# Optimization experiments

Measured on AMD Instinct MI355X. Metric: run time of the kernel, lower is better.

## Reference

```python
import jax, jax.numpy as jnp
import numpy as np

L = 3        # num_layers
B = 8192     # batch slots
H = 1024     # hidden_dim (== decoder_in_dim)
D_IN = 1024
D_OUT = 80
N_ACT = 4096 # active rows selected by hidden_idx


def setup_inputs() -> dict:
    key = jax.random.key(0)
    ks = jax.random.split(key, 8)
    encoded = jax.random.normal(ks[0], (B, D_IN), jnp.float32)
    hidden = jax.random.normal(ks[1], (L, B, H), jnp.float32)
    hidden_idx = jnp.arange(N_ACT, dtype=jnp.int32)  # unique, in-range batch indices
    s = 0.05  # small init scale for stable gate math
    w_ih = jax.random.normal(ks[2], (L, 3 * H, D_IN), jnp.float32) * s
    w_hh = jax.random.normal(ks[3], (L, 3 * H, H), jnp.float32) * s
    b_ih = jax.random.normal(ks[4], (L, 3 * H), jnp.float32) * s
    b_hh = jax.random.normal(ks[5], (L, 3 * H), jnp.float32) * s
    w_out = jax.random.normal(ks[6], (D_OUT, H), jnp.float32) * s
    b_out = jax.random.normal(ks[7], (D_OUT,), jnp.float32) * s
    return {"encoded": encoded, "hidden": hidden, "hidden_idx": hidden_idx,
            "w_ih": w_ih, "w_hh": w_hh, "b_ih": b_ih, "b_hh": b_hh,
            "w_out": w_out, "b_out": b_out}


def reference(encoded, hidden, hidden_idx, w_ih, w_hh, b_ih, b_hh, w_out, b_out):
    # Gather active rows, run stacked GRUCells, scatter back (eval mode: dropout = identity).
    x = encoded[hidden_idx]                       # [N, D_IN]
    new_hidden = []
    for i in range(L):                            # small fixed layer loop
        h_full = hidden[i]                        # [B, H]
        h = h_full[hidden_idx]                    # [N, H]
        gi = x @ w_ih[i].T + b_ih[i]              # [N, 3H] gates from input
        gh = h @ w_hh[i].T + b_hh[i]              # [N, 3H] gates from hidden
        i_r, i_z, i_n = jnp.split(gi, 3, axis=-1)
        h_r, h_z, h_n = jnp.split(gh, 3, axis=-1)
        r = jax.nn.sigmoid(i_r + h_r)
        z = jax.nn.sigmoid(i_z + h_z)
        n = jnp.tanh(i_n + r * h_n)
        h_out = (1.0 - z) * n + z * h             # torch GRUCell update
        x = h_out
        new_hidden.append(h_full.at[hidden_idx].set(h_out))
    y = jnp.tanh(x @ w_out.T + b_out)             # linear head + tanh activation
    output = jnp.zeros((B, D_OUT), y.dtype).at[hidden_idx].set(y)
    return (output, jnp.stack(new_hidden))
```

## Files before the change

### kernel.cpp

```cpp
#include <hip/hip_runtime.h>

typedef unsigned short ushort_t;
typedef unsigned char uchar_t;
typedef unsigned int uint_t;
typedef __attribute__((ext_vector_type(8))) short bf16x8;
typedef __attribute__((ext_vector_type(4))) float f32x4;

constexpr int L_   = 3;
constexpr int B_   = 8192;
constexpr int H_   = 1024;
constexpr int DOUT_= 80;
constexpr int NACT_= 4096;
constexpr int G3_  = 3 * H_;

static __device__ __forceinline__ ushort_t f2bf(float f) {
    uint_t u = __float_as_uint(f);
    uint_t r = (u + 0x7FFFu + ((u >> 16) & 1u)) >> 16;
    return (ushort_t)r;
}

static __device__ __forceinline__ void gll16(const void* g, void* l) {
    __builtin_amdgcn_global_load_lds(
        (const __attribute__((address_space(1))) uint32_t*)g,
        (__attribute__((address_space(3))) uint32_t*)l, 16, 0, 0);
}

__global__ void prep_all(const float* __restrict__ encoded, const float* __restrict__ hidden,
                         const int* __restrict__ idx,
                         const float* __restrict__ wih, const float* __restrict__ whh,
                         const float* __restrict__ wout,
                         ushort_t* __restrict__ oih, ushort_t* __restrict__ ohh,
                         ushort_t* __restrict__ oout,
                         ushort_t* __restrict__ x0, ushort_t* __restrict__ hb,
                         uchar_t* __restrict__ mask) {
    int tid = blockIdx.x * blockDim.x + threadIdx.x;
    int nth = gridDim.x * blockDim.x;
    if (tid < NACT_) mask[idx[tid]] = 1;
    const int NW = L_ * G3_ * H_ / 4;
    for (int i = tid; i < NW; i += nth) {
        float4 a = ((const float4*)wih)[i];
        ushort4 o; o.x = f2bf(a.x); o.y = f2bf(a.y); o.z = f2bf(a.z); o.w = f2bf(a.w);
        ((ushort4*)oih)[i] = o;
        float4 b = ((const float4*)whh)[i];
        ushort4 p; p.x = f2bf(b.x); p.y = f2bf(b.y); p.z = f2bf(b.z); p.w = f2bf(b.w);
        ((ushort4*)ohh)[i] = p;
    }
    const int NO = DOUT_ * H_ / 4;
    for (int i = tid; i < NO; i += nth) {
        float4 a = ((const float4*)wout)[i];
        ushort4 o; o.x = f2bf(a.x); o.y = f2bf(a.y); o.z = f2bf(a.z); o.w = f2bf(a.w);
        ((ushort4*)oout)[i] = o;
    }
    const int C4 = H_ / 4;
    const int PER = NACT_ * C4;
    for (int i = tid; i < 4 * PER; i += nth) {
        int seg = i / PER;
        int rem = i - seg * PER;
        int r = rem / C4, c = rem % C4;
        int gr = idx[r];
        const float* src = (seg == 0) ? (encoded + (size_t)gr * H_)
                                      : (hidden + ((size_t)(seg - 1) * B_ + gr) * H_);
        float4 v = ((const float4*)src)[c];
        ushort4 o; o.x = f2bf(v.x); o.y = f2bf(v.y); o.z = f2bf(v.z); o.w = f2bf(v.w);
        ushort_t* dst = (seg == 0) ? x0 : (hb + (size_t)(seg - 1) * NACT_ * H_);
        ((ushort4*)(dst + (size_t)r * H_))[c] = o;
    }
}

__global__ __launch_bounds__(256, 2) void gru_layer(
    const ushort_t* __restrict__ xb,
    const ushort_t* __restrict__ hb,
    const float* __restrict__ hid_full,
    const ushort_t* __restrict__ wih,
    const ushort_t* __restrict__ whh,
    const float* __restrict__ bih, const float* __restrict__ bhh,
    const int* __restrict__ idx,
    float* __restrict__ out_hid,
    ushort_t* __restrict__ xnext,
    const uchar_t* __restrict__ mask)
{
    __shared__ ushort_t As[128 * 64];
    __shared__ ushort_t Ws[192 * 64];

    const int tid = threadIdx.x;
    const int bid = blockIdx.x;
    const int swz = (bid & 7) * 64 + (bid >> 3);
    const int bn = swz & 15, bm = swz >> 4;
    const int row0 = bm * 128, col0 = bn * 64;
    const int wave = tid >> 6, lane = tid & 63;
    const int wr = wave >> 1, wc = wave & 1;
    const int fl = lane & 15, fh = lane >> 4;
    const int srow = lane >> 3;
    const int sxor = ((lane & 7) ^ srow) * 8;

    f32x4 accR[4][2] = {};
    f32x4 accZ[4][2] = {};
    f32x4 accN[2][4][2] = {};

#pragma unroll
    for (int ph = 0; ph < 2; ++ph) {
        const ushort_t* Asrc = ph ? hb : xb;
        const ushort_t* Wsrc = ph ? whh : wih;
        const ushort_t* abase[4];
        const ushort_t* wbase[6];
#pragma unroll
        for (int t = 0; t < 4; ++t)
            abase[t] = Asrc + (size_t)(row0 + wave * 32 + t * 8 + srow) * H_ + sxor;
#pragma unroll
        for (int t = 0; t < 6; ++t) {
            const int slot = wave * 48 + t * 8 + srow;
            const int gate = slot >> 6, rowW = slot & 63;
            wbase[t] = Wsrc + (size_t)(gate * H_ + col0 + rowW) * H_ + sxor;
        }
        for (int kk = 0; kk < H_; kk += 64) {
            __syncthreads();
#pragma unroll
            for (int t = 0; t < 4; ++t)
                gll16(abase[t] + kk, &As[wave * 2048 + t * 512]);
#pragma unroll
            for (int t = 0; t < 6; ++t)
                gll16(wbase[t] + kk, &Ws[wave * 3072 + t * 512]);
            __syncthreads();
#pragma unroll
            for (int ks = 0; ks < 2; ++ks) {
                const int sl = ((ks * 4 + fh) ^ (fl & 7)) * 8;
                bf16x8 a[4];
#pragma unroll
                for (int m = 0; m < 4; ++m)
                    a[m] = *(const bf16x8*)&As[(wr * 64 + m * 16 + fl) * 64 + sl];
#pragma unroll
                for (int g = 0; g < 3; ++g) {
#pragma unroll
                    for (int n = 0; n < 2; ++n) {
                        const bf16x8 b = *(const bf16x8*)&Ws[(g * 64 + wc * 32 + n * 16 + fl) * 64 + sl];
#pragma unroll
                        for (int m = 0; m < 4; ++m) {
                            if (g == 0)
                                accR[m][n] = __builtin_amdgcn_mfma_f32_16x16x32_bf16(a[m], b, accR[m][n], 0, 0, 0);
                            else if (g == 1)
                                accZ[m][n] = __builtin_amdgcn_mfma_f32_16x16x32_bf16(a[m], b, accZ[m][n], 0, 0, 0);
                            else
                                accN[ph][m][n] = __builtin_amdgcn_mfma_f32_16x16x32_bf16(a[m], b, accN[ph][m][n], 0, 0, 0);
                        }
                    }
                }
            }
        }
    }

#pragma unroll
    for (int m = 0; m < 4; ++m) {
#pragma unroll
        for (int n = 0; n < 2; ++n) {
            const int c = col0 + wc * 32 + n * 16 + fl;
            const float br_r = bih[c] + bhh[c];
            const float br_z = bih[H_ + c] + bhh[H_ + c];
            const float bi_n = bih[2 * H_ + c];
            const float bh_n = bhh[2 * H_ + c];
#pragma unroll
            for (int j = 0; j < 4; ++j) {
                const int r = row0 + wr * 64 + m * 16 + fh * 4 + j;
                const float vr = 1.f / (1.f + expf(-(accR[m][n][j] + br_r)));
                const float vz = 1.f / (1.f + expf(-(accZ[m][n][j] + br_z)));
                const float vn = tanhf(accN[0][m][n][j] + bi_n + vr * (accN[1][m][n][j] + bh_n));
                const int gr = idx[r];
                const float h0 = hid_full[(size_t)gr * H_ + c];
                const float ho = (1.f - vz) * vn + vz * h0;
                out_hid[(size_t)gr * H_ + c] = ho;
                xnext[(size_t)r * H_ + c] = f2bf(ho);
            }
        }
    }

    const int tot = B_ * (H_ / 4);
    for (int i = bid * 256 + tid; i < tot; i += 512 * 256) {
        const int row = i >> 8;
        if (!mask[row]) ((float4*)out_hid)[i] = ((const float4*)hid_full)[i];
    }
}

__global__ __launch_bounds__(256) void head_gemm(
    const ushort_t* __restrict__ xb, const ushort_t* __restrict__ wo,
    const float* __restrict__ bo, const int* __restrict__ idx,
    float* __restrict__ outy)
{
    __shared__ ushort_t Xs[64][72];
    __shared__ ushort_t Ws[80][72];
    const int tid = threadIdx.x;
    const int row0 = blockIdx.x * 64;
    const int lrow = tid >> 2, lseg = tid & 3;
    const int wave = tid >> 6, lane = tid & 63;
    const int fl = lane & 15, fh = lane >> 4;
    f32x4 acc[5] = {};

    for (int kk = 0; kk < H_; kk += 64) {
        __syncthreads();
        const ushort_t* xp = xb + (size_t)(row0 + lrow) * H_ + kk + lseg * 16;
        *(uint4*)&Xs[lrow][lseg * 16]     = *(const uint4*)xp;
        *(uint4*)&Xs[lrow][lseg * 16 + 8] = *(const uint4*)(xp + 8);
        for (int t = tid; t < 320; t += 256) {
            int r = t >> 2, s = t & 3;
            const ushort_t* wp = wo + (size_t)r * H_ + kk + s * 16;
            *(uint4*)&Ws[r][s * 16]     = *(const uint4*)wp;
            *(uint4*)&Ws[r][s * 16 + 8] = *(const uint4*)(wp + 8);
        }
        __syncthreads();
#pragma unroll
        for (int ks = 0; ks < 64; ks += 32) {
            bf16x8 a = *(const bf16x8*)&Xs[wave * 16 + fl][ks + fh * 8];
#pragma unroll
            for (int nf = 0; nf < 5; ++nf) {
                bf16x8 b = *(const bf16x8*)&Ws[nf * 16 + fl][ks + fh * 8];
                acc[nf] = __builtin_amdgcn_mfma_f32_16x16x32_bf16(a, b, acc[nf], 0, 0, 0);
            }
        }
    }
#pragma unroll
    for (int nf = 0; nf < 5; ++nf) {
        const int c = nf * 16 + fl;
        const float bb = bo[c];
#pragma unroll
        for (int j = 0; j < 4; ++j) {
            const int r = row0 + wave * 16 + fh * 4 + j;
            const float y = tanhf(acc[nf][j] + bb);
            outy[(size_t)idx[r] * DOUT_ + c] = y;
        }
    }
}

extern "C" void kernel_launch(void* const* d_in, const int* in_sizes, int n_in,
                              void* d_out, int out_size, void* d_ws, size_t ws_size,
                              hipStream_t stream) {
    const float* encoded = (const float*)d_in[0];
    const float* hidden  = (const float*)d_in[1];
    const int*   idx     = (const int*)d_in[2];
    const float* w_ih    = (const float*)d_in[3];
    const float* w_hh    = (const float*)d_in[4];
    const float* b_ih    = (const float*)d_in[5];
    const float* b_hh    = (const float*)d_in[6];
    const float* w_out   = (const float*)d_in[7];
    const float* b_out   = (const float*)d_in[8];

    float* outy = (float*)d_out;
    float* outh = outy + (size_t)B_ * DOUT_;

    ushort_t* ws    = (ushort_t*)d_ws;
    ushort_t* wihb  = ws;
    ushort_t* whhb  = wihb + (size_t)L_ * G3_ * H_;
    ushort_t* woutb = whhb + (size_t)L_ * G3_ * H_;
    ushort_t* xb0   = woutb + (size_t)DOUT_ * H_;
    ushort_t* xb1   = xb0 + (size_t)NACT_ * H_;
    ushort_t* hb    = xb1 + (size_t)NACT_ * H_;
    uchar_t*  mask  = (uchar_t*)(hb + (size_t)L_ * NACT_ * H_);

    hipMemsetAsync(outy, 0, (size_t)B_ * DOUT_ * sizeof(float), stream);
    hipMemsetAsync(mask, 0, B_, stream);
    prep_all<<<2048, 256, 0, stream>>>(encoded, hidden, idx, w_ih, w_hh, w_out,
                                       wihb, whhb, woutb, xb0, hb, mask);

    ushort_t* xin = xb0;
    ushort_t* xout = xb1;
    for (int i = 0; i < L_; ++i) {
        gru_layer<<<512, 256, 0, stream>>>(
            xin, hb + (size_t)i * NACT_ * H_, hidden + (size_t)i * B_ * H_,
            wihb + (size_t)i * G3_ * H_, whhb + (size_t)i * G3_ * H_,
            b_ih + (size_t)i * G3_, b_hh + (size_t)i * G3_, idx,
            outh + (size_t)i * B_ * H_, xout, mask);
        ushort_t* t = xin; xin = xout; xout = t;
    }
    head_gemm<<<64, 256, 0, stream>>>(xin, woutb, b_out, idx, outy);
}
```

Measured before the change: 300.3 us.

## Double-buffer GRU GEMM K-loop and split inactive-row copy into its own kernel

Moves the GRU layer GEMM to double-buffered LDS: the tile for step k+1 is prefetched with global_load_lds while MFMAs run on step k, using vmcnt waits and raw s_barrier, and the prefetch spans the switch from the input phase to the hidden phase. The per-layer copy of inactive hidden rows is pulled out of the GEMM kernel into one separate copy_inactive kernel covering all layers. The aim is to hide global load latency behind compute and to shorten the GEMM kernel's tail. In exchange LDS use doubles to 80KB per block, which may cut the two-blocks-per-CU occupancy requested by the launch bounds, and the hand-written waitcnt logic is fragile.

```diff
diff --git a/kernel.cpp b/kernel.cpp
--- a/kernel.cpp
+++ b/kernel.cpp
@@ -67,6 +67,78 @@
     }
 }
 
+__global__ void copy_inactive(const float* __restrict__ hidden, const uchar_t* __restrict__ mask,
+                              float* __restrict__ outh) {
+    const int total = L_ * B_ * (H_ / 4);
+    int i = blockIdx.x * blockDim.x + threadIdx.x;
+    int nth = gridDim.x * blockDim.x;
+    for (; i < total; i += nth) {
+        int row = (i >> 8) & (B_ - 1);
+        if (mask[row]) continue;
+        ((float4*)outh)[i] = ((const float4*)hidden)[i];
+    }
+}
+
+template<bool LAST>
+static __device__ __forceinline__ void gru_sweep(
+    const ushort_t* __restrict__ cA, const ushort_t* __restrict__ cW,
+    const ushort_t* __restrict__ nA, const ushort_t* __restrict__ nW,
+    const uint_t* aoff, const uint_t* woff,
+    ushort_t* lds0, ushort_t* lds1,
+    int wave, int wr, int wc, int fl, int fh,
+    f32x4 (&accR)[4][2], f32x4 (&accZ)[4][2], f32x4 (&accN)[4][2])
+{
+#pragma unroll 2
+    for (int kki = 0; kki < 16; ++kki) {
+        ushort_t* rb = (kki & 1) ? lds1 : lds0;
+        ushort_t* sb = (kki & 1) ? lds0 : lds1;
+        if (kki < 15) {
+#pragma unroll
+            for (int t = 0; t < 4; ++t) gll16(cA + aoff[t] + (kki + 1) * 64, sb + wave * 2048 + t * 512);
+#pragma unroll
+            for (int t = 0; t < 6; ++t) gll16(cW + woff[t] + (kki + 1) * 64, sb + 8192 + wave * 3072 + t * 512);
+            asm volatile("s_waitcnt vmcnt(10)" ::: "memory");
+        } else if (!LAST) {
+#pragma unroll
+            for (int t = 0; t < 4; ++t) gll16(nA + aoff[t], sb + wave * 2048 + t * 512);
+#pragma unroll
+            for (int t = 0; t < 6; ++t) gll16(nW + woff[t], sb + 8192 + wave * 3072 + t * 512);
+            asm volatile("s_waitcnt vmcnt(10)" ::: "memory");
+        } else {
+            asm volatile("s_waitcnt vmcnt(0)" ::: "memory");
+        }
+        __builtin_amdgcn_s_barrier();
+        asm volatile("" ::: "memory");
+        __builtin_amdgcn_sched_barrier(0);
+#pragma unroll
+        for (int ks = 0; ks < 2; ++ks) {
+            const int sl = ((ks * 4 + fh) ^ (fl & 7)) * 8;
+            bf16x8 a[4];
+#pragma unroll
+            for (int m = 0; m < 4; ++m)
+                a[m] = *(const bf16x8*)&rb[(wr * 64 + m * 16 + fl) * 64 + sl];
+#pragma unroll
+            for (int g = 0; g < 3; ++g) {
+#pragma unroll
+                for (int n = 0; n < 2; ++n) {
+                    const bf16x8 b = *(const bf16x8*)&rb[8192 + (g * 64 + wc * 32 + n * 16 + fl) * 64 + sl];
+#pragma unroll
+                    for (int m = 0; m < 4; ++m) {
+                        if (g == 0)
+                            accR[m][n] = __builtin_amdgcn_mfma_f32_16x16x32_bf16(a[m], b, accR[m][n], 0, 0, 0);
+                        else if (g == 1)
+                            accZ[m][n] = __builtin_amdgcn_mfma_f32_16x16x32_bf16(a[m], b, accZ[m][n], 0, 0, 0);
+                        else
+                            accN[m][n] = __builtin_amdgcn_mfma_f32_16x16x32_bf16(a[m], b, accN[m][n], 0, 0, 0);
+                    }
+                }
+            }
+        }
+        __builtin_amdgcn_sched_barrier(0);
+        __builtin_amdgcn_s_barrier();
+    }
+}
+
 __global__ __launch_bounds__(256, 2) void gru_layer(
     const ushort_t* __restrict__ xb,
     const ushort_t* __restrict__ hb,
@@ -76,11 +148,9 @@
     const float* __restrict__ bih, const float* __restrict__ bhh,
     const int* __restrict__ idx,
     float* __restrict__ out_hid,
-    ushort_t* __restrict__ xnext,
-    const uchar_t* __restrict__ mask)
+    ushort_t* __restrict__ xnext)
 {
-    __shared__ ushort_t As[128 * 64];
-    __shared__ ushort_t Ws[192 * 64];
+    __shared__ ushort_t lds[2][20480];
 
     const int tid = threadIdx.x;
     const int bid = blockIdx.x;
@@ -93,60 +163,30 @@
     const int srow = lane >> 3;
     const int sxor = ((lane & 7) ^ srow) * 8;
 
+    uint_t aoff[4], woff[6];
+#pragma unroll
+    for (int t = 0; t < 4; ++t)
+        aoff[t] = (uint_t)(row0 + wave * 32 + t * 8 + srow) * H_ + sxor;
+#pragma unroll
+    for (int t = 0; t < 6; ++t) {
+        const int slot = wave * 48 + t * 8 + srow;
+        woff[t] = (uint_t)((slot >> 6) * H_ + col0 + (slot & 63)) * H_ + sxor;
+    }
+
     f32x4 accR[4][2] = {};
     f32x4 accZ[4][2] = {};
-    f32x4 accN[2][4][2] = {};
-
-#pragma unroll
-    for (int ph = 0; ph < 2; ++ph) {
-        const ushort_t* Asrc = ph ? hb : xb;
-        const ushort_t* Wsrc = ph ? whh : wih;
-        const ushort_t* abase[4];
-        const ushort_t* wbase[6];
-#pragma unroll
-        for (int t = 0; t < 4; ++t)
-            abase[t] = Asrc + (size_t)(row0 + wave * 32 + t * 8 + srow) * H_ + sxor;
-#pragma unroll
-        for (int t = 0; t < 6; ++t) {
-            const int slot = wave * 48 + t * 8 + srow;
-            const int gate = slot >> 6, rowW = slot & 63;
-            wbase[t] = Wsrc + (size_t)(gate * H_ + col0 + rowW) * H_ + sxor;
-        }
-        for (int kk = 0; kk < H_; kk += 64) {
-            __syncthreads();
-#pragma unroll
-            for (int t = 0; t < 4; ++t)
-                gll16(abase[t] + kk, &As[wave * 2048 + t * 512]);
-#pragma unroll
-            for (int t = 0; t < 6; ++t)
-                gll16(wbase[t] + kk, &Ws[wave * 3072 + t * 512]);
-            __syncthreads();
-#pragma unroll
-            for (int ks = 0; ks < 2; ++ks) {
-                const int sl = ((ks * 4 + fh) ^ (fl & 7)) * 8;
-                bf16x8 a[4];
-#pragma unroll
-                for (int m = 0; m < 4; ++m)
-                    a[m] = *(const bf16x8*)&As[(wr * 64 + m * 16 + fl) * 64 + sl];
-#pragma unroll
-                for (int g = 0; g < 3; ++g) {
-#pragma unroll
-                    for (int n = 0; n < 2; ++n) {
-                        const bf16x8 b = *(const bf16x8*)&Ws[(g * 64 + wc * 32 + n * 16 + fl) * 64 + sl];
-#pragma unroll
-                        for (int m = 0; m < 4; ++m) {
-                            if (g == 0)
-                                accR[m][n] = __builtin_amdgcn_mfma_f32_16x16x32_bf16(a[m], b, accR[m][n], 0, 0, 0);
-                            else if (g == 1)
-                                accZ[m][n] = __builtin_amdgcn_mfma_f32_16x16x32_bf16(a[m], b, accZ[m][n], 0, 0, 0);
-                            else
-                                accN[ph][m][n] = __builtin_amdgcn_mfma_f32_16x16x32_bf16(a[m], b, accN[ph][m][n], 0, 0, 0);
-                        }
-                    }
-                }
-            }
-        }
-    }
+    f32x4 accNx[4][2] = {};
+    f32x4 accNh[4][2] = {};
+
+#pragma unroll
+    for (int t = 0; t < 4; ++t) gll16(xb + aoff[t], lds[0] + wave * 2048 + t * 512);
+#pragma unroll
+    for (int t = 0; t < 6; ++t) gll16(wih + woff[t], lds[0] + 8192 + wave * 3072 + t * 512);
+
+    gru_sweep<false>(xb, wih, hb, whh, aoff, woff, lds[0], lds[1],
+                     wave, wr, wc, fl, fh, accR, accZ, accNx);
+    gru_sweep<true >(hb, whh, nullptr, nullptr, aoff, woff, lds[0], lds[1],
+                     wave, wr, wc, fl, fh, accR, accZ, accNh);
 
 #pragma unroll
     for (int m = 0; m < 4; ++m) {
@@ -162,7 +202,7 @@
                 const int r = row0 + wr * 64 + m * 16 + fh * 4 + j;
                 const float vr = 1.f / (1.f + expf(-(accR[m][n][j] + br_r)));
                 const float vz = 1.f / (1.f + expf(-(accZ[m][n][j] + br_z)));
-                const float vn = tanhf(accN[0][m][n][j] + bi_n + vr * (accN[1][m][n][j] + bh_n));
+                const float vn = tanhf(accNx[m][n][j] + bi_n + vr * (accNh[m][n][j] + bh_n));
                 const int gr = idx[r];
                 const float h0 = hid_full[(size_t)gr * H_ + c];
                 const float ho = (1.f - vz) * vn + vz * h0;
@@ -170,12 +210,6 @@
                 xnext[(size_t)r * H_ + c] = f2bf(ho);
             }
         }
-    }
-
-    const int tot = B_ * (H_ / 4);
-    for (int i = bid * 256 + tid; i < tot; i += 512 * 256) {
-        const int row = i >> 8;
-        if (!mask[row]) ((float4*)out_hid)[i] = ((const float4*)hid_full)[i];
     }
 }
 
@@ -257,6 +291,7 @@
     hipMemsetAsync(mask, 0, B_, stream);
     prep_all<<<2048, 256, 0, stream>>>(encoded, hidden, idx, w_ih, w_hh, w_out,
                                        wihb, whhb, woutb, xb0, hb, mask);
+    copy_inactive<<<2048, 256, 0, stream>>>(hidden, mask, outh);
 
     ushort_t* xin = xb0;
     ushort_t* xout = xb1;
@@ -265,7 +300,7 @@
             xin, hb + (size_t)i * NACT_ * H_, hidden + (size_t)i * B_ * H_,
             wihb + (size_t)i * G3_ * H_, whhb + (size_t)i * G3_ * H_,
             b_ih + (size_t)i * G3_, b_hh + (size_t)i * G3_, idx,
-            outh + (size_t)i * B_ * H_, xout, mask);
+            outh + (size_t)i * B_ * H_, xout);
         ushort_t* t = xin; xin = xout; xout = t;
     }
     head_gemm<<<64, 256, 0, stream>>>(xin, woutb, b_out, idx, outy);
```

Measured after the change: 279.1 us. 1.08x faster.
